# Optimization experiments

Hardware: AMD Instinct MI355X
Metric: run time of the kernel (lower is better)

## Reference

```python
import jax, jax.numpy as jnp
import numpy as np


def _conv(x, w, b):
    # NCHW conv, SAME padding for odd kernel, stride 1
    pad = (w.shape[2] - 1) // 2
    y = jax.lax.conv_general_dilated(
        x, w, window_strides=(1, 1), padding=[(pad, pad), (pad, pad)],
        dimension_numbers=('NCHW', 'OIHW', 'NCHW'))
    return y + b[None, :, None, None]


def _cell(x, h, c, m, p):
    # one TransGRU cell step; x:[B,Cin,H,W], h/c/m:[B,hc,H,W]
    A = _conv(jnp.concatenate([x, h], axis=1), p['w_rzo'], p['b_rzo'])   # [B,3hc,H,W]
    Bm = _conv(jnp.concatenate([x, m], axis=1), p['w_rz'], p['b_rz'])    # [B,2hc,H,W]
    decay_h = jnp.exp(-p['td_h'])[None]          # (1,hc,1,1)
    decay_m = jnp.exp(-p['td_m'])[None]
    gate = jax.nn.sigmoid(p['tg'])[None]
    Ar, Az, Ao = jnp.split(A, 3, axis=1)
    Br, Bz = jnp.split(Bm, 2, axis=1)
    r = jax.nn.sigmoid(Ar * gate + h * decay_h)
    z = jax.nn.sigmoid(Az * gate + h * decay_h)
    o = jax.nn.sigmoid(Ao)
    xr = jax.nn.sigmoid(Br * gate + m * decay_m)
    xz = jax.nn.sigmoid(Bz * gate + m * decay_m)
    gc = jnp.tanh(_conv(jnp.concatenate([x, r * c], axis=1), p['w_h'], p['b_h']))
    gm = jnp.tanh(_conv(jnp.concatenate([x, xr * m], axis=1), p['w_h'], p['b_h']))
    c_new = z * c + (1 - z) * gc
    m_new = xz * m + (1 - xz) * gm
    h_new = o * jnp.tanh(_conv(jnp.concatenate([c_new, m_new], axis=1), p['w_o'], p['b_o']))
    return h_new, c_new, m_new, (r, z, xr, xz, c_new, m_new, gc, gm, o)


def _forward(x, params, attention_size):
    B, T, _, H, W = x.shape
    L = len(params)
    hcs = [p['w_rzo'].shape[0] // 3 for p in params]
    hc_last = hcs[-1]
    dtype = x.dtype
    init_states = tuple(
        tuple(jnp.zeros((B, hc, H, W), dtype) for _ in range(3)) for hc in hcs)
    init_gates = tuple(jnp.zeros((B, hc_last, H, W), dtype) for _ in range(9))

    def step(carry, xt):
        states, _ = carry
        inp = xt
        m = states[-1][2]  # layer 0 reads m from last layer of previous step
        new_states = []
        gates = None
        for l in range(L):
            h, c, _own_m = states[l]
            inp, cn, mn, gates = _cell(inp, h, c, m, params[l])
            new_states.append((inp, cn, mn))
            m = mn  # next layer reads m just produced by this layer
        return (tuple(new_states), gates), inp

    (final_states, gates), hs = jax.lax.scan(
        step, (init_states, init_gates), jnp.swapaxes(x, 0, 1))
    # gates from last layer at final step (matches torch leaking loop vars)
    r, z, xr, xz, c, m, gc, gm, o = gates
    q = ((r + xr + c + gc) * 0.25).reshape(B, hc_last, H * W)
    k = ((r + xr + m + gm) * 0.25).reshape(B, hc_last, H * W)
    v = jnp.swapaxes(hs, 0, 1).reshape(B, T, hc_last, H * W)
    scale = 1.0 / float(np.sqrt(attention_size))
    attn = jax.nn.softmax(jnp.einsum('bcn,bdn->bcd', q, k) * scale, axis=-1)
    out = jnp.einsum('bcd,btdn->btcn', attn, v).reshape(B, T, hc_last, H, W)
    return out


def setup_inputs() -> dict:
    key = jax.random.key(0)
    ks = jax.random.split(key, 32)
    d = {'x': jax.random.normal(ks[0], (4, 8, 16, 64, 64), jnp.float32)}
    specs = {
        'w_rzo0': (192, 80, 3, 3), 'b_rzo0': (192,), 'w_rz0': (128, 80, 3, 3),
        'b_rz0': (128,), 'w_h0': (64, 80, 3, 3), 'b_h0': (64,),
        'w_o0': (64, 128, 1, 1), 'b_o0': (64,), 'td_h0': (64, 1, 1),
        'td_m0': (64, 1, 1), 'tg0': (64, 1, 1),
        'w_rzo1': (192, 128, 3, 3), 'b_rzo1': (192,), 'w_rz1': (128, 128, 3, 3),
        'b_rz1': (128,), 'w_h1': (64, 128, 3, 3), 'b_h1': (64,),
        'w_o1': (64, 128, 1, 1), 'b_o1': (64,), 'td_h1': (64, 1, 1),
        'td_m1': (64, 1, 1), 'tg1': (64, 1, 1),
    }
    for i, (name, shp) in enumerate(specs.items()):
        d[name] = jax.random.normal(ks[i + 1], shp, jnp.float32) * 0.05
    d['attention_size'] = 4096
    return d


def reference(x, w_rzo0, b_rzo0, w_rz0, b_rz0, w_h0, b_h0, w_o0, b_o0,
              td_h0, td_m0, tg0, w_rzo1, b_rzo1, w_rz1, b_rz1, w_h1, b_h1,
              w_o1, b_o1, td_h1, td_m1, tg1, attention_size):
    params = [
        dict(w_rzo=w_rzo0, b_rzo=b_rzo0, w_rz=w_rz0, b_rz=b_rz0, w_h=w_h0,
             b_h=b_h0, w_o=w_o0, b_o=b_o0, td_h=td_h0, td_m=td_m0, tg=tg0),
        dict(w_rzo=w_rzo1, b_rzo=b_rzo1, w_rz=w_rz1, b_rz=b_rz1, w_h=w_h1,
             b_h=b_h1, w_o=w_o1, b_o=b_o1, td_h=td_h1, td_m=td_m1, tg=tg1),
    ]
    return _forward(x, params, attention_size)
```

## Files before the change

### kernel.cpp

```cpp
#include <hip/hip_runtime.h>
#include <math.h>

#define HWN 4096
#define Bn 4
#define Tn 8

typedef __attribute__((ext_vector_type(8))) _Float16 f16x8;
typedef __attribute__((ext_vector_type(4))) float floatx4;

__device__ __forceinline__ float sigmoidf_(float v) { return 1.f / (1.f + expf(-v)); }

__device__ __forceinline__ void split8(const float* vv, f16x8* hi, f16x8* lo) {
#pragma unroll
    for (int j = 0; j < 8; ++j) {
        _Float16 h = (_Float16)vv[j];
        (*hi)[j] = h;
        (*lo)[j] = (_Float16)(vv[j] - (float)h);
    }
}

__global__ __launch_bounds__(256) void prep_w_kernel(
    const float* __restrict__ W, _Float16* __restrict__ dst,
    int Ctot, int Cout, int nch, int KK)
{
    const int ncog = Cout >> 4;
    const long total = (long)KK * nch * ncog * 512;
    for (long i = (long)blockIdx.x * 256 + threadIdx.x; i < total;
         i += (long)gridDim.x * 256) {
        int j    = (int)(i & 7);
        int lane = (int)((i >> 3) & 63);
        long r   = i >> 9;
        int f = (int)(r % ncog); r /= ncog;
        int c = (int)(r % nch);  r /= nch;
        int kk = (int)r;
        int co = f * 16 + (lane & 15);
        int ci = c * 32 + (lane >> 4) * 8 + j;
        float v = (ci < Ctot) ? W[((long)co * Ctot + ci) * KK + kk] : 0.f;
        _Float16 hi = (_Float16)v;
        dst[i]         = hi;
        dst[total + i] = (_Float16)(v - (float)hi);
    }
}

__global__ __launch_bounds__(256) void prep_x_kernel(
    const float* __restrict__ x, float* __restrict__ xcl)
{
    const int i = blockIdx.x * 256 + threadIdx.x;
    const int px = i & 4095;
    const int t  = (i >> 12) & 7;
    const int b  = i >> 15;
    float* d = xcl + (((long)t * Bn + b) * HWN + px) * 16;
#pragma unroll
    for (int ch = 0; ch < 16; ++ch)
        d[ch] = x[((long)(b * 8 + t) * 16 + ch) * HWN + px];
}

template<int EPI, int NF>
__global__ __launch_bounds__(256) void conv3m(
    const float* __restrict__ in1, int C1,
    const float* __restrict__ in2a, const float* __restrict__ in2b,
    int Ctot, int nch,
    const _Float16* __restrict__ wA, const float* __restrict__ biasA,
    float* outA, int CoutA, int ncogA,
    const _Float16* __restrict__ wB, const float* __restrict__ biasB,
    float* outB, int CoutB, int ncogB, int nA,
    const float* zA, const float* zB,
    const float* sA, const float* sB,
    const float* rten, const float* xrten,
    float* qout, float* kout, int last)
{
    __shared__ __align__(16) _Float16 ldsB[18][18][2][40];

    const int tid = threadIdx.x;
    const int ty0 = (blockIdx.x >> 2) * 16;
    const int tx0 = (blockIdx.x & 3) * 16;
    const int b   = blockIdx.z & 3;
    const int which = (EPI == 1) ? (int)(blockIdx.z >> 2)
                                 : (blockIdx.y >= (unsigned)nA ? 1 : 0);

    const float*    in2  = which ? in2b : in2a;
    const _Float16* Wf   = which ? wB : wA;
    const float*    bias = which ? biasB : biasA;
    float*          outp = which ? outB : outA;
    const int Cout = which ? CoutB : CoutA;
    const int ncog = which ? ncogB : ncogA;
    const int cog0 = (EPI == 1) ? blockIdx.y * NF
                   : (which ? (blockIdx.y - nA) * NF : blockIdx.y * NF);
    const int co0  = cog0 * 16;

    const int lane = tid & 63, wv = tid >> 6, tl = lane & 15, quad = lane >> 4;
    const int C2 = Ctot - C1;
    const long wplane = (long)9 * nch * ncog * 512;
    const float* in1b  = in1 + (long)b * HWN * C1;
    const float* in2bb = in2 + (long)b * HWN * C2;

    floatx4 acc[NF][4];
#pragma unroll
    for (int f = 0; f < NF; ++f)
#pragma unroll
        for (int g = 0; g < 4; ++g) acc[f][g] = (floatx4){0.f, 0.f, 0.f, 0.f};

    float4 pa[6], pb[6];
    auto prefetch = [&](int c) {
        const int c0 = c * 32;
#pragma unroll
        for (int s = 0; s < 6; ++s) {
            const int i = tid + s * 256;
            float4 va = {0.f, 0.f, 0.f, 0.f}, vb = {0.f, 0.f, 0.f, 0.f};
            if (i < 1296) {
                const int pxh = i >> 2, cig = i & 3;
                const int yh = pxh / 18, xh = pxh - yh * 18;
                const int y = ty0 + yh - 1, x = tx0 + xh - 1;
                const int ch = c0 + cig * 8;
                if (ch < Ctot && (unsigned)y < 64u && (unsigned)x < 64u) {
                    const float* src; long off;
                    if (ch < C1) { src = in1b;  off = (long)(y * 64 + x) * C1 + ch; }
                    else         { src = in2bb; off = (long)(y * 64 + x) * C2 + ch - C1; }
                    va = *(const float4*)(src + off);
                    vb = *(const float4*)(src + off + 4);
                }
            }
            pa[s] = va; pb[s] = vb;
        }
    };

    prefetch(0);

    for (int c = 0; c < nch; ++c) {
        f16x8 wh[2][NF], wl[2][NF];
        {
            const long wo0 = ((long)(0 * nch + c) * ncog + cog0) * 512 + lane * 8;
#pragma unroll
            for (int f = 0; f < NF; ++f) {
                wh[0][f] = *(const f16x8*)(Wf + wo0 + (long)f * 512);
                wl[0][f] = *(const f16x8*)(Wf + wplane + wo0 + (long)f * 512);
            }
        }

        __syncthreads();
#pragma unroll
        for (int s = 0; s < 6; ++s) {
            const int i = tid + s * 256;
            if (i < 1296) {
                const int pxh = i >> 2, cig = i & 3;
                const int yh = pxh / 18, xh = pxh - yh * 18;
                float vv[8] = {pa[s].x, pa[s].y, pa[s].z, pa[s].w,
                               pb[s].x, pb[s].y, pb[s].z, pb[s].w};
                f16x8 vh, vl;
                split8(vv, &vh, &vl);
                *(f16x8*)&ldsB[yh][xh][0][cig * 8] = vh;
                *(f16x8*)&ldsB[yh][xh][1][cig * 8] = vl;
            }
        }
        __syncthreads();
        if (c + 1 < nch) prefetch(c + 1);

#pragma unroll
        for (int kx = 0; kx < 3; ++kx) {
            f16x8 rh[6], rl[6];
#pragma unroll
            for (int rr = 0; rr < 6; ++rr) {
                const _Float16* pB = &ldsB[wv * 4 + rr][tl + kx][0][quad * 8];
                rh[rr] = *(const f16x8*)pB;
                rl[rr] = *(const f16x8*)(pB + 40);
            }
#pragma unroll
            for (int ky = 0; ky < 3; ++ky) {
                const int s = kx * 3 + ky;
                const int cur = s & 1, nxt = cur ^ 1;
                if (s < 8) {
                    const int sn  = s + 1;
                    const int kxn = sn / 3, kyn = sn - kxn * 3;
                    const int kkn = kyn * 3 + kxn;
                    const long wo = ((long)(kkn * nch + c) * ncog + cog0) * 512 + lane * 8;
#pragma unroll
                    for (int f = 0; f < NF; ++f) {
                        wh[nxt][f] = *(const f16x8*)(Wf + wo + (long)f * 512);
                        wl[nxt][f] = *(const f16x8*)(Wf + wplane + wo + (long)f * 512);
                    }
                }
#pragma unroll
                for (int f = 0; f < NF; ++f)
#pragma unroll
                    for (int g = 0; g < 4; ++g) {
                        acc[f][g] = __builtin_amdgcn_mfma_f32_16x16x32_f16(wh[cur][f], rh[g + ky], acc[f][g], 0, 0, 0);
                        acc[f][g] = __builtin_amdgcn_mfma_f32_16x16x32_f16(wh[cur][f], rl[g + ky], acc[f][g], 0, 0, 0);
                        acc[f][g] = __builtin_amdgcn_mfma_f32_16x16x32_f16(wl[cur][f], rh[g + ky], acc[f][g], 0, 0, 0);
                    }
            }
        }
    }

    if (EPI == 0) {
        const long obb = (long)b * HWN * Cout;
#pragma unroll
        for (int f = 0; f < NF; ++f) {
            const int co = co0 + f * 16 + quad * 4;
#pragma unroll
            for (int g = 0; g < 4; ++g) {
                const long px = (long)(ty0 + wv * 4 + g) * 64 + tx0 + tl;
                float4 v;
                v.x = acc[f][g][0] + bias[co + 0];
                v.y = acc[f][g][1] + bias[co + 1];
                v.z = acc[f][g][2] + bias[co + 2];
                v.w = acc[f][g][3] + bias[co + 3];
                *(float4*)(outp + obb + px * Cout + co) = v;
            }
        }
    } else {
        const float* zt = which ? zB : zA;
        const float* st = which ? sB : sA;
        float* qk = which ? kout : qout;
#pragma unroll
        for (int f = 0; f < NF; ++f) {
            const int co = co0 + f * 16 + quad * 4;
#pragma unroll
            for (int g = 0; g < 4; ++g) {
                const long px = (long)(ty0 + wv * 4 + g) * 64 + tx0 + tl;
                const long off = (long)b * HWN * 64 + px * 64 + co;
                float4 zv = *(const float4*)(zt + off);
                float4 sv = *(const float4*)(st + off);
                float gv[4], cn[4];
                gv[0] = tanhf(acc[f][g][0] + bias[co + 0]);
                gv[1] = tanhf(acc[f][g][1] + bias[co + 1]);
                gv[2] = tanhf(acc[f][g][2] + bias[co + 2]);
                gv[3] = tanhf(acc[f][g][3] + bias[co + 3]);
                cn[0] = zv.x * sv.x + (1.f - zv.x) * gv[0];
                cn[1] = zv.y * sv.y + (1.f - zv.y) * gv[1];
                cn[2] = zv.z * sv.z + (1.f - zv.z) * gv[2];
                cn[3] = zv.w * sv.w + (1.f - zv.w) * gv[3];
                *(float4*)(outp + off) = *(float4*)cn;
                if (last) {
                    float4 rv = *(const float4*)(rten + off);
                    float4 xv = *(const float4*)(xrten + off);
                    qk[((long)(b * 64) + co + 0) * HWN + px] = 0.25f * (rv.x + xv.x + cn[0] + gv[0]);
                    qk[((long)(b * 64) + co + 1) * HWN + px] = 0.25f * (rv.y + xv.y + cn[1] + gv[1]);
                    qk[((long)(b * 64) + co + 2) * HWN + px] = 0.25f * (rv.z + xv.z + cn[2] + gv[2]);
                    qk[((long)(b * 64) + co + 3) * HWN + px] = 0.25f * (rv.w + xv.w + cn[3] + gv[3]);
                }
            }
        }
    }
}

__global__ __launch_bounds__(256) void conv1x1m(
    const float* __restrict__ cten, const float* __restrict__ mten,
    const float* __restrict__ oten,
    const _Float16* __restrict__ W, const float* __restrict__ bias,
    float* houtp)
{
    const int tid = threadIdx.x;
    const int lane = tid & 63, wv = tid >> 6, tl = lane & 15, quad = lane >> 4;
    const int b = blockIdx.y;
    const int px = blockIdx.x * 64 + wv * 16 + tl;
    const long bb = (long)b * HWN * 64;

    f16x8 wh[4][4], wl[4][4];
#pragma unroll
    for (int c = 0; c < 4; ++c)
#pragma unroll
        for (int f = 0; f < 4; ++f) {
            const long wo = (long)(c * 4 + f) * 512 + lane * 8;
            wh[c][f] = *(const f16x8*)(W + wo);
            wl[c][f] = *(const f16x8*)(W + 8192 + wo);
        }
    f16x8 bh[4], bl[4];
#pragma unroll
    for (int c = 0; c < 4; ++c) {
        const float* src = (c < 2) ? cten : mten;
        const int ch0 = (c & 1) * 32 + quad * 8;
        const long off = bb + (long)px * 64 + ch0;
        float4 p0 = *(const float4*)(src + off);
        float4 p1 = *(const float4*)(src + off + 4);
        float vv[8] = {p0.x, p0.y, p0.z, p0.w, p1.x, p1.y, p1.z, p1.w};
        split8(vv, &bh[c], &bl[c]);
    }

    floatx4 acc[4];
#pragma unroll
    for (int f = 0; f < 4; ++f) acc[f] = (floatx4){0.f, 0.f, 0.f, 0.f};
#pragma unroll
    for (int c = 0; c < 4; ++c)
#pragma unroll
        for (int f = 0; f < 4; ++f) {
            acc[f] = __builtin_amdgcn_mfma_f32_16x16x32_f16(wh[c][f], bh[c], acc[f], 0, 0, 0);
            acc[f] = __builtin_amdgcn_mfma_f32_16x16x32_f16(wh[c][f], bl[c], acc[f], 0, 0, 0);
            acc[f] = __builtin_amdgcn_mfma_f32_16x16x32_f16(wl[c][f], bh[c], acc[f], 0, 0, 0);
        }

#pragma unroll
    for (int f = 0; f < 4; ++f) {
        const int co = f * 16 + quad * 4;
        const long off = bb + (long)px * 64 + co;
        float4 ov = *(const float4*)(oten + off);
        float4 hv;
        hv.x = ov.x * tanhf(acc[f][0] + bias[co + 0]);
        hv.y = ov.y * tanhf(acc[f][1] + bias[co + 1]);
        hv.z = ov.z * tanhf(acc[f][2] + bias[co + 2]);
        hv.w = ov.w * tanhf(acc[f][3] + bias[co + 3]);
        *(float4*)(houtp + off) = hv;
    }
}

__global__ __launch_bounds__(256) void gates_cl(
    const float* __restrict__ A, const float* __restrict__ Bm,
    const float* __restrict__ h, const float* __restrict__ m,
    const float* __restrict__ c,
    const float* __restrict__ td_h, const float* __restrict__ td_m,
    const float* __restrict__ tg,
    float* r, float* xr, float* z, float* xz,
    float* o, float* rc, float* xm)
{
    const int i  = blockIdx.x * 256 + threadIdx.x;
    const int ch = (i & 15) * 4;
    const long px = (i >> 4) & 4095;
    const int b  = i >> 16;
    const long b64  = ((long)b * HWN + px) * 64 + ch;
    const long b192 = ((long)b * HWN + px) * 192 + ch;
    const long b128 = ((long)b * HWN + px) * 128 + ch;

    float4 Ar = *(const float4*)(A + b192);
    float4 Az = *(const float4*)(A + b192 + 64);
    float4 Ao = *(const float4*)(A + b192 + 128);
    float4 Br = *(const float4*)(Bm + b128);
    float4 Bz = *(const float4*)(Bm + b128 + 64);
    float4 hv = *(const float4*)(h + b64);
    float4 mv = *(const float4*)(m + b64);
    float4 cv = *(const float4*)(c + b64);

    float rv[4], zv[4], ov[4], xrv[4], xzv[4], rcv[4], xmv[4];
    const float* Arp = (const float*)&Ar; const float* Azp = (const float*)&Az;
    const float* Aop = (const float*)&Ao; const float* Brp = (const float*)&Br;
    const float* Bzp = (const float*)&Bz; const float* hp = (const float*)&hv;
    const float* mp = (const float*)&mv;  const float* cp = (const float*)&cv;
#pragma unroll
    for (int j = 0; j < 4; ++j) {
        const float g  = sigmoidf_(tg[ch + j]);
        const float dh = expf(-td_h[ch + j]);
        const float dm = expf(-td_m[ch + j]);
        rv[j]  = sigmoidf_(Arp[j] * g + hp[j] * dh);
        zv[j]  = sigmoidf_(Azp[j] * g + hp[j] * dh);
        ov[j]  = sigmoidf_(Aop[j]);
        xrv[j] = sigmoidf_(Brp[j] * g + mp[j] * dm);
        xzv[j] = sigmoidf_(Bzp[j] * g + mp[j] * dm);
        rcv[j] = rv[j] * cp[j];
        xmv[j] = xrv[j] * mp[j];
    }
    *(float4*)(r  + b64) = *(float4*)rv;
    *(float4*)(xr + b64) = *(float4*)xrv;
    *(float4*)(z  + b64) = *(float4*)zv;
    *(float4*)(xz + b64) = *(float4*)xzv;
    *(float4*)(o  + b64) = *(float4*)ov;
    *(float4*)(rc + b64) = *(float4*)rcv;
    *(float4*)(xm + b64) = *(float4*)xmv;
}

__global__ __launch_bounds__(256) void logits_part(
    const float* __restrict__ q, const float* __restrict__ k, float* __restrict__ part)
{
    __shared__ float qs[64][66], ks[64][66];
    const int tid = threadIdx.x;
    const int b = blockIdx.x, kc = blockIdx.y;
    const int cqq = tid >> 4, ckq = tid & 15;
    float pacc[4][4];
#pragma unroll
    for (int u = 0; u < 4; ++u)
#pragma unroll
        for (int v = 0; v < 4; ++v) pacc[u][v] = 0.f;

    for (int sub = 0; sub < 4; ++sub) {
        const int px0 = kc * 256 + sub * 64;
        __syncthreads();
#pragma unroll
        for (int rr = 0; rr < 16; ++rr) {
            const int idx = rr * 256 + tid;
            const int chh = idx >> 6, pxo = idx & 63;
            qs[chh][pxo] = q[((long)b * 64 + chh) * HWN + px0 + pxo];
            ks[chh][pxo] = k[((long)b * 64 + chh) * HWN + px0 + pxo];
        }
        __syncthreads();
        for (int p = 0; p < 64; ++p) {
            float qv[4], kv[4];
#pragma unroll
            for (int u = 0; u < 4; ++u) { qv[u] = qs[cqq + 16 * u][p]; kv[u] = ks[ckq + 16 * u][p]; }
#pragma unroll
            for (int u = 0; u < 4; ++u)
#pragma unroll
                for (int v = 0; v < 4; ++v) pacc[u][v] = fmaf(qv[u], kv[v], pacc[u][v]);
        }
    }
#pragma unroll
    for (int u = 0; u < 4; ++u)
#pragma unroll
        for (int v = 0; v < 4; ++v)
            part[(((long)b * 16 + kc) * 64 + cqq + 16 * u) * 64 + ckq + 16 * v] = pacc[u][v];
}

__global__ void reduce_softmax(const float* __restrict__ part, float* __restrict__ attn)
{
    const int row = blockIdx.x;
    const int b = row >> 6, cq = row & 63;
    const int lane = threadIdx.x;
    float s = 0.f;
#pragma unroll
    for (int kc = 0; kc < 16; ++kc)
        s += part[(((long)b * 16 + kc) * 64 + cq) * 64 + lane];
    float v = s * (1.f / 64.f);
    float mx = v;
    for (int off = 32; off; off >>= 1) mx = fmaxf(mx, __shfl_xor(mx, off));
    float e = expf(v - mx);
    float sum = e;
    for (int off = 32; off; off >>= 1) sum += __shfl_xor(sum, off);
    attn[row * 64 + lane] = e / sum;
}

__global__ __launch_bounds__(256) void out_cl(
    const float* __restrict__ attn, const float* __restrict__ hs,
    float* __restrict__ outp)
{
    __shared__ __align__(16) float att_t[64][8];
    const int bt = blockIdx.x;
    const int b = bt >> 3, t = bt & 7;
    const int c0 = blockIdx.z * 8;
    const int tid = threadIdx.x;
    for (int i = tid; i < 512; i += 256) {
        int d = i >> 3, j = i & 7;
        att_t[d][j] = attn[(b * 64 + c0 + j) * 64 + d];
    }
    __syncthreads();

    const long px = blockIdx.y * 256 + tid;
    const long SLOT = (long)Bn * HWN * 64;
    const float* vb = hs + (long)t * SLOT + ((long)b * HWN + px) * 64;

    float acc[8];
#pragma unroll
    for (int j = 0; j < 8; ++j) acc[j] = 0.f;
#pragma unroll 4
    for (int dg = 0; dg < 16; ++dg) {
        float4 v4 = *(const float4*)(vb + dg * 4);
        const float* vp = (const float*)&v4;
#pragma unroll
        for (int j4 = 0; j4 < 4; ++j4) {
            const float vv = vp[j4];
            const float4 a0 = *(const float4*)&att_t[dg * 4 + j4][0];
            const float4 a1 = *(const float4*)&att_t[dg * 4 + j4][4];
            acc[0] = fmaf(vv, a0.x, acc[0]); acc[1] = fmaf(vv, a0.y, acc[1]);
            acc[2] = fmaf(vv, a0.z, acc[2]); acc[3] = fmaf(vv, a0.w, acc[3]);
            acc[4] = fmaf(vv, a1.x, acc[4]); acc[5] = fmaf(vv, a1.y, acc[5]);
            acc[6] = fmaf(vv, a1.z, acc[6]); acc[7] = fmaf(vv, a1.w, acc[7]);
        }
    }
    const long ob = ((long)(b * 8 + t) * 64 + c0) * HWN + px;
#pragma unroll
    for (int j = 0; j < 8; ++j) outp[ob + (long)j * HWN] = acc[j];
}

extern "C" void kernel_launch(void* const* d_in, const int* in_sizes, int n_in,
                              void* d_out, int out_size, void* d_ws, size_t ws_size,
                              hipStream_t stream)
{
    const float* x = (const float*)d_in[0];
    const float* w_rzo[2] = {(const float*)d_in[1],  (const float*)d_in[12]};
    const float* b_rzo[2] = {(const float*)d_in[2],  (const float*)d_in[13]};
    const float* w_rz[2]  = {(const float*)d_in[3],  (const float*)d_in[14]};
    const float* b_rz[2]  = {(const float*)d_in[4],  (const float*)d_in[15]};
    const float* w_h[2]   = {(const float*)d_in[5],  (const float*)d_in[16]};
    const float* b_h[2]   = {(const float*)d_in[6],  (const float*)d_in[17]};
    const float* w_o[2]   = {(const float*)d_in[7],  (const float*)d_in[18]};
    const float* b_o[2]   = {(const float*)d_in[8],  (const float*)d_in[19]};
    const float* td_h[2]  = {(const float*)d_in[9],  (const float*)d_in[20]};
    const float* td_m[2]  = {(const float*)d_in[10], (const float*)d_in[21]};
    const float* tg[2]    = {(const float*)d_in[11], (const float*)d_in[22]};

    const size_t S64 = (size_t)Bn * HWN * 64;
    float* P = (float*)d_ws;
    float* h0    = P; P += S64;
    float* c0    = P; P += S64;
    float* m0    = P; P += S64;
    float* c1    = P; P += S64;
    float* m1    = P; P += S64;
    float* zslab = P; P += S64;
    float* A_cl  = P; P += (size_t)Bn * HWN * 192;
    float* B_cl  = P; P += (size_t)Bn * HWN * 128;
    float* rb    = P; P += S64;
    float* xrb   = P; P += S64;
    float* zb    = P; P += S64;
    float* xzb   = P; P += S64;
    float* ogb   = P; P += S64;
    float* rcb   = P; P += S64;
    float* xmb   = P; P += S64;
    float* hs    = P; P += (size_t)Tn * S64;
    float* x_cl  = P; P += (size_t)Tn * Bn * HWN * 16;
    _Float16* wA0 = (_Float16*)P;
    _Float16* wB0 = wA0 + 331776;
    _Float16* wH0 = wB0 + 221184;
    _Float16* wA1 = wH0 + 110592;
    _Float16* wB1 = wA1 + 442368;
    _Float16* wH1 = wB1 + 294912;
    _Float16* wO0 = wH1 + 147456;
    _Float16* wO1 = wO0 + 16384;
    float* qbuf  = A_cl;
    float* kbuf  = qbuf + S64;
    float* partb = kbuf + S64;
    float* attnb = partb + (size_t)Bn * 16 * 64 * 64;

    hipMemsetAsync(h0, 0, 6 * S64 * sizeof(float), stream);

    prep_x_kernel<<<512, 256, 0, stream>>>(x, x_cl);
    prep_w_kernel<<<128, 256, 0, stream>>>(w_rzo[0], wA0, 80, 192, 3, 9);
    prep_w_kernel<<<128, 256, 0, stream>>>(w_rz[0],  wB0, 80, 128, 3, 9);
    prep_w_kernel<<<128, 256, 0, stream>>>(w_h[0],   wH0, 80,  64, 3, 9);
    prep_w_kernel<<<128, 256, 0, stream>>>(w_rzo[1], wA1, 128, 192, 4, 9);
    prep_w_kernel<<<128, 256, 0, stream>>>(w_rz[1],  wB1, 128, 128, 4, 9);
    prep_w_kernel<<<128, 256, 0, stream>>>(w_h[1],   wH1, 128, 64, 4, 9);
    prep_w_kernel<<<64, 256, 0, stream>>>(w_o[0], wO0, 128, 64, 4, 1);
    prep_w_kernel<<<64, 256, 0, stream>>>(w_o[1], wO1, 128, 64, 4, 1);

    for (int t = 0; t < Tn; ++t) {
        const float* xt = x_cl + (size_t)t * Bn * HWN * 16;
        const float* h1prev = (t == 0) ? zslab : (hs + (size_t)(t - 1) * S64);
        float* h1out = hs + (size_t)t * S64;

        conv3m<0, 2><<<dim3(16, 10, 4), 256, 0, stream>>>(
            xt, 16, h0, m1, 80, 3,
            wA0, b_rzo[0], A_cl, 192, 12,
            wB0, b_rz[0],  B_cl, 128, 8, 6,
            nullptr, nullptr, nullptr, nullptr, nullptr, nullptr, nullptr, nullptr, 0);
        gates_cl<<<1024, 256, 0, stream>>>(A_cl, B_cl, h0, m1, c0,
            td_h[0], td_m[0], tg[0], rb, xrb, zb, xzb, ogb, rcb, xmb);
        conv3m<1, 1><<<dim3(16, 4, 8), 256, 0, stream>>>(
            xt, 16, rcb, xmb, 80, 3,
            wH0, b_h[0], c0, 64, 4,
            wH0, b_h[0], m0, 64, 4, 0,
            zb, xzb, c0, m1, rb, xrb, qbuf, kbuf, 0);
        conv1x1m<<<dim3(64, 4), 256, 0, stream>>>(c0, m0, ogb, wO0, b_o[0], h0);

        conv3m<0, 2><<<dim3(16, 10, 4), 256, 0, stream>>>(
            h0, 64, h1prev, m0, 128, 4,
            wA1, b_rzo[1], A_cl, 192, 12,
            wB1, b_rz[1],  B_cl, 128, 8, 6,
            nullptr, nullptr, nullptr, nullptr, nullptr, nullptr, nullptr, nullptr, 0);
        gates_cl<<<1024, 256, 0, stream>>>(A_cl, B_cl, h1prev, m0, c1,
            td_h[1], td_m[1], tg[1], rb, xrb, zb, xzb, ogb, rcb, xmb);
        conv3m<1, 1><<<dim3(16, 4, 8), 256, 0, stream>>>(
            h0, 64, rcb, xmb, 128, 4,
            wH1, b_h[1], c1, 64, 4,
            wH1, b_h[1], m1, 64, 4, 0,
            zb, xzb, c1, m0, rb, xrb, qbuf, kbuf, (t == Tn - 1) ? 1 : 0);
        conv1x1m<<<dim3(64, 4), 256, 0, stream>>>(c1, m1, ogb, wO1, b_o[1], h1out);
    }

    logits_part<<<dim3(4, 16), 256, 0, stream>>>(qbuf, kbuf, partb);
    reduce_softmax<<<256, 64, 0, stream>>>(partb, attnb);
    out_cl<<<dim3(32, 16, 8), 256, 0, stream>>>(attnb, hs, (float*)d_out);
}
```

Baseline: 1.454 ms.

## Deepen weight prefetch to three buffers, delay input prefetch, repack LDS rows

Weight fragments are now loaded two taps ahead using a triple buffer instead of one tap ahead with a double buffer, to hide global-load latency behind more MFMAs. The prefetch of the next channel chunk's input tile moves from right after the LDS store to after the second kx column, spreading memory traffic across the compute loop. The LDS tile drops the hi/lo plane dimension for a single padded row of 72 halves, which changes bank mapping. The extra buffer adds register pressure, which may reduce occupancy or cause spills.

```diff
diff --git a/kernel.cpp b/kernel.cpp
--- a/kernel.cpp
+++ b/kernel.cpp
@@ -69,7 +69,7 @@
     const float* rten, const float* xrten,
     float* qout, float* kout, int last)
 {
-    __shared__ __align__(16) _Float16 ldsB[18][18][2][40];
+    __shared__ __align__(16) _Float16 ldsB[18][18][72];
 
     const int tid = threadIdx.x;
     const int ty0 = (blockIdx.x >> 2) * 16;
@@ -127,15 +127,19 @@
     prefetch(0);
 
     for (int c = 0; c < nch; ++c) {
-        f16x8 wh[2][NF], wl[2][NF];
-        {
-            const long wo0 = ((long)(0 * nch + c) * ncog + cog0) * 512 + lane * 8;
-#pragma unroll
-            for (int f = 0; f < NF; ++f) {
-                wh[0][f] = *(const f16x8*)(Wf + wo0 + (long)f * 512);
-                wl[0][f] = *(const f16x8*)(Wf + wplane + wo0 + (long)f * 512);
-            }
-        }
+        f16x8 wh[3][NF], wl[3][NF];
+#define LOADW(S, BUF)                                                           \
+        {                                                                       \
+            const int kk_ = ((S) % 3) * 3 + (S) / 3;                            \
+            const long wo_ = ((long)(kk_ * nch + c) * ncog + cog0) * 512 + lane * 8; \
+            _Pragma("unroll")                                                   \
+            for (int f = 0; f < NF; ++f) {                                      \
+                wh[BUF][f] = *(const f16x8*)(Wf + wo_ + (long)f * 512);         \
+                wl[BUF][f] = *(const f16x8*)(Wf + wplane + wo_ + (long)f * 512);\
+            }                                                                   \
+        }
+        LOADW(0, 0)
+        LOADW(1, 1)
 
         __syncthreads();
 #pragma unroll
@@ -148,37 +152,26 @@
                                pb[s].x, pb[s].y, pb[s].z, pb[s].w};
                 f16x8 vh, vl;
                 split8(vv, &vh, &vl);
-                *(f16x8*)&ldsB[yh][xh][0][cig * 8] = vh;
-                *(f16x8*)&ldsB[yh][xh][1][cig * 8] = vl;
+                *(f16x8*)&ldsB[yh][xh][cig * 8]      = vh;
+                *(f16x8*)&ldsB[yh][xh][40 + cig * 8] = vl;
             }
         }
         __syncthreads();
-        if (c + 1 < nch) prefetch(c + 1);
 
 #pragma unroll
         for (int kx = 0; kx < 3; ++kx) {
             f16x8 rh[6], rl[6];
 #pragma unroll
             for (int rr = 0; rr < 6; ++rr) {
-                const _Float16* pB = &ldsB[wv * 4 + rr][tl + kx][0][quad * 8];
+                const _Float16* pB = &ldsB[wv * 4 + rr][tl + kx][quad * 8];
                 rh[rr] = *(const f16x8*)pB;
                 rl[rr] = *(const f16x8*)(pB + 40);
             }
 #pragma unroll
             for (int ky = 0; ky < 3; ++ky) {
                 const int s = kx * 3 + ky;
-                const int cur = s & 1, nxt = cur ^ 1;
-                if (s < 8) {
-                    const int sn  = s + 1;
-                    const int kxn = sn / 3, kyn = sn - kxn * 3;
-                    const int kkn = kyn * 3 + kxn;
-                    const long wo = ((long)(kkn * nch + c) * ncog + cog0) * 512 + lane * 8;
-#pragma unroll
-                    for (int f = 0; f < NF; ++f) {
-                        wh[nxt][f] = *(const f16x8*)(Wf + wo + (long)f * 512);
-                        wl[nxt][f] = *(const f16x8*)(Wf + wplane + wo + (long)f * 512);
-                    }
-                }
+                if (s < 7) LOADW(s + 2, (s + 2) % 3)
+                const int cur = s % 3;
 #pragma unroll
                 for (int f = 0; f < NF; ++f)
 #pragma unroll
@@ -188,7 +181,9 @@
                         acc[f][g] = __builtin_amdgcn_mfma_f32_16x16x32_f16(wl[cur][f], rh[g + ky], acc[f][g], 0, 0, 0);
                     }
             }
-        }
+            if (kx == 1 && c + 1 < nch) prefetch(c + 1);
+        }
+#undef LOADW
     }
 
     if (EPI == 0) {
```

Result: faster. 1.379 ms (-5.2%).
